# Kernel tuning notes

Measured on AMD Instinct MI355X. Metric: run time of the kernel, lower is better.

## Reference

```python
import jax, jax.numpy as jnp
import numpy as np
import math

D = 512
B, L = 8, 2048
EPS = 1e-5

def setup_inputs() -> dict:
    key = jax.random.key(0)
    ks = jax.random.split(key, 8)
    s = 1.0 / math.sqrt(D)
    x = jax.random.normal(ks[0], (B, L, D), dtype=jnp.float32)
    adj = jax.random.randint(ks[1], (B, L, L), 0, 2, dtype=jnp.int32)
    Wq = jax.random.normal(ks[2], (D, D), dtype=jnp.float32) * s
    Wk = jax.random.normal(ks[3], (D, D), dtype=jnp.float32) * s
    Wv = jax.random.normal(ks[4], (D, D), dtype=jnp.float32) * s
    Wo = jax.random.normal(ks[5], (D, D), dtype=jnp.float32) * s
    bo = jnp.zeros((D,), dtype=jnp.float32)
    gamma = jnp.ones((D,), dtype=jnp.float32)
    beta = jnp.zeros((D,), dtype=jnp.float32)
    return {"x": x, "adj": adj, "Wq": Wq, "Wk": Wk, "Wv": Wv,
            "Wo": Wo, "bo": bo, "gamma": gamma, "beta": beta}

def layer_norm(y, gamma, beta):
    mu = jnp.mean(y, axis=-1, keepdims=True)
    var = jnp.mean(jnp.square(y - mu), axis=-1, keepdims=True)
    return (y - mu) * jax.lax.rsqrt(var + EPS) * gamma + beta

def reference(x, adj, Wq, Wk, Wv, Wo, bo, gamma, beta):
    d_out = Wq.shape[1]
    scale = 1.0 / math.sqrt(d_out)
    Q = x @ Wq                          # [B,L,D]
    K = x @ Wk
    V = x @ Wv
    sc = jnp.einsum('bld,bmd->blm', Q, K) * scale   # [B,L,L]
    mask = adj == 0
    sc = jnp.where(mask, -jnp.inf, sc)
    all_inf = jnp.all(mask, axis=-1, keepdims=True)  # rows with no neighbors
    sc = jnp.where(all_inf, 0.0, sc)                 # -> uniform attention
    w = jax.nn.softmax(sc, axis=-1)                  # dropout off (eval)
    out = jnp.einsum('blm,bmd->bld', w, V)
    y = x + out @ Wo + bo
    return layer_norm(y, gamma, beta)
```

## Files before the change

kernel.cpp:

```cpp
#include <hip/hip_runtime.h>
#include <hip/hip_bf16.h>

typedef short bf16x8 __attribute__((ext_vector_type(8)));
typedef float f32x4  __attribute__((ext_vector_type(4)));
typedef unsigned int u32;

#define LSEQ 2048
#define DDIM 512
#define NBAT 8

__device__ __forceinline__ void gld_lds16(const __hip_bfloat16* g, __hip_bfloat16* l) {
    __builtin_amdgcn_global_load_lds(
        (const __attribute__((address_space(1))) u32*)g,
        (__attribute__((address_space(3))) u32*)l, 16, 0, 0);
}

__global__ void k_cvt_x(const float* __restrict__ x, __hip_bfloat16* __restrict__ xb) {
    size_t i = ((size_t)blockIdx.x * 256 + threadIdx.x) * 4;
    float4 v = *(const float4*)(x + i);
    __hip_bfloat16 h[4] = { __float2bfloat16(v.x), __float2bfloat16(v.y),
                            __float2bfloat16(v.z), __float2bfloat16(v.w) };
    *(short4*)(xb + i) = *(short4*)h;
}

__global__ void k_cvt_w(const float* __restrict__ Wq, const float* __restrict__ Wk,
                        const float* __restrict__ Wv, const float* __restrict__ Wo,
                        __hip_bfloat16* __restrict__ Wtqkv, __hip_bfloat16* __restrict__ Wto) {
    __shared__ float t[32][33];
    int mat = blockIdx.x >> 8;
    int tb  = blockIdx.x & 255;
    int tk  = tb >> 4, tn = tb & 15;
    const float* W = (mat == 0) ? Wq : (mat == 1) ? Wk : (mat == 2) ? Wv : Wo;
    int c  = threadIdx.x & 31;
    int r0 = threadIdx.x >> 5;
#pragma unroll
    for (int i = 0; i < 4; ++i) {
        int r = r0 + i * 8;
        t[r][c] = W[(size_t)(tk * 32 + r) * 512 + tn * 32 + c];
    }
    __syncthreads();
    __hip_bfloat16* dst = (mat < 3) ? (Wtqkv + (size_t)mat * 512 * 512) : Wto;
#pragma unroll
    for (int i = 0; i < 4; ++i) {
        int n = r0 + i * 8;
        dst[(size_t)(tn * 32 + n) * 512 + tk * 32 + c] = __float2bfloat16(t[c][n]);
    }
}

__global__ __launch_bounds__(256, 2)
void k_gemm_qkv(const __hip_bfloat16* __restrict__ A, const __hip_bfloat16* __restrict__ Bt,
                __hip_bfloat16* __restrict__ Q, __hip_bfloat16* __restrict__ Kb,
                __hip_bfloat16* __restrict__ Vt) {
    __shared__ __hip_bfloat16 As[128][32], Bs[128][32];
    const int tid = threadIdx.x, lane = tid & 63, w = tid >> 6;
    const int l15 = lane & 15, l4 = lane >> 4;
    const int mt = blockIdx.x, nt = blockIdx.y;
    const int wr = (w >> 1) * 64, wc = (w & 1) * 64;
    const int sr = lane >> 2, so = (lane & 3) * 8;
    f32x4 acc[4][4] = {};

#pragma unroll 1
    for (int kt = 0; kt < 16; ++kt) {
        __syncthreads();
#pragma unroll
        for (int i = 0; i < 2; ++i) {
            int r0 = w * 32 + i * 16;
            gld_lds16(A  + (size_t)(mt * 128 + r0 + sr) * 512 + kt * 32 + so, &As[r0][0]);
            gld_lds16(Bt + (size_t)(nt * 128 + r0 + sr) * 512 + kt * 32 + so, &Bs[r0][0]);
        }
        __syncthreads();
        bf16x8 af[4], bfr[4];
#pragma unroll
        for (int i = 0; i < 4; ++i)
            af[i] = *(const bf16x8*)(&As[wr + 16 * i + l15][l4 * 8]);
#pragma unroll
        for (int j = 0; j < 4; ++j)
            bfr[j] = *(const bf16x8*)(&Bs[wc + 16 * j + l15][l4 * 8]);
        __builtin_amdgcn_s_setprio(1);
#pragma unroll
        for (int i = 0; i < 4; ++i)
#pragma unroll
            for (int j = 0; j < 4; ++j)
                acc[i][j] = __builtin_amdgcn_mfma_f32_16x16x32_bf16(af[i], bfr[j], acc[i][j], 0, 0, 0);
        __builtin_amdgcn_s_setprio(0);
    }
    const int which = (nt * 128) >> 9;
#pragma unroll
    for (int i = 0; i < 4; ++i) {
#pragma unroll
        for (int r = 0; r < 4; ++r) {
            int grow = mt * 128 + wr + 16 * i + (l4 << 2) + r;
#pragma unroll
            for (int j = 0; j < 4; ++j) {
                int gcol = nt * 128 + wc + 16 * j + l15;
                int cc = gcol & 511;
                __hip_bfloat16 h = __float2bfloat16(acc[i][j][r]);
                if (which == 0)      Q [(size_t)grow * 512 + cc] = h;
                else if (which == 1) Kb[(size_t)grow * 512 + cc] = h;
                else {
                    int b = grow >> 11, m = grow & 2047;
                    Vt[((size_t)b * 512 + cc) * 2048 + m] = h;
                }
            }
        }
    }
}

__global__ __launch_bounds__(512, 2)
void k_attn(const __hip_bfloat16* __restrict__ Q, const __hip_bfloat16* __restrict__ Kg,
            const __hip_bfloat16* __restrict__ Vt, const int* __restrict__ adj,
            __hip_bfloat16* __restrict__ P0, __hip_bfloat16* __restrict__ P1,
            float* __restrict__ mlb) {
    __shared__ __hip_bfloat16 Kl[2][32][520];
    __shared__ __hip_bfloat16 Vl[2][512][32];
    __shared__ __hip_bfloat16 Pl[8][16][40];
    const int tid = threadIdx.x, lane = tid & 63, w = tid >> 6;
    const int l15 = lane & 15, l4 = lane >> 4;
    const int b = blockIdx.x & 7, qt = (blockIdx.x >> 3) & 15, s = blockIdx.x >> 7;
    const float scale = 0.04419417382415922f;
    __hip_bfloat16* __restrict__ Op = s ? P1 : P0;

    const __hip_bfloat16* kbase = Kg + ((size_t)b * LSEQ + s * 1024) * 512;
    const __hip_bfloat16* vbase = Vt + (size_t)b * 512 * 2048 + s * 1024;
    const int* abase = adj + ((size_t)b * LSEQ + qt * 128 + w * 16 + l4 * 4) * LSEQ + s * 1024 + l15;
    const int vsr = lane >> 2, vso = (lane & 3) * 8;

    bf16x8 qf[16];
    {
        const __hip_bfloat16* qp = Q + ((size_t)b * LSEQ + qt * 128 + w * 16 + l15) * 512;
#pragma unroll
        for (int ks = 0; ks < 16; ++ks)
            qf[ks] = *(const bf16x8*)(qp + ks * 32 + l4 * 8);
    }
    f32x4 acc[32];
#pragma unroll
    for (int n = 0; n < 32; ++n) acc[n] = (f32x4){0.f, 0.f, 0.f, 0.f};
    float m_[4] = {-1e30f, -1e30f, -1e30f, -1e30f};
    float l_[4] = {0.f, 0.f, 0.f, 0.f};

    int adjv[8];
    {
#pragma unroll
        for (int i = 0; i < 4; ++i) {
            int r = w + i * 8;
            gld_lds16(kbase + (size_t)r * 512 + lane * 8, &Kl[0][r][0]);
        }
#pragma unroll
        for (int i = 0; i < 4; ++i) {
            int r0 = (w * 4 + i) * 16;
            gld_lds16(vbase + (size_t)(r0 + vsr) * 2048 + vso, &Vl[0][r0][0]);
        }
#pragma unroll
        for (int r = 0; r < 4; ++r)
#pragma unroll
            for (int n = 0; n < 2; ++n)
                adjv[r * 2 + n] = abase[(size_t)r * LSEQ + n * 16];
    }
    __syncthreads();

#pragma unroll 1
    for (int t = 0; t < 32; ++t) {
        const int cur = t & 1, nxt = cur ^ 1;
        unsigned amask = 0;
#pragma unroll
        for (int r = 0; r < 4; ++r)
#pragma unroll
            for (int n = 0; n < 2; ++n)
                amask |= (adjv[r * 2 + n] != 0 ? 1u : 0u) << (n * 4 + r);
        if (t < 31) {
            const __hip_bfloat16* kp = kbase + (size_t)(t + 1) * 32 * 512;
#pragma unroll
            for (int i = 0; i < 4; ++i) {
                int r = w + i * 8;
                gld_lds16(kp + (size_t)r * 512 + lane * 8, &Kl[nxt][r][0]);
            }
            const __hip_bfloat16* vp = vbase + (t + 1) * 32;
#pragma unroll
            for (int i = 0; i < 4; ++i) {
                int r0 = (w * 4 + i) * 16;
                gld_lds16(vp + (size_t)(r0 + vsr) * 2048 + vso, &Vl[nxt][r0][0]);
            }
            const int* ap = abase + (t + 1) * 32;
#pragma unroll
            for (int r = 0; r < 4; ++r)
#pragma unroll
                for (int n = 0; n < 2; ++n)
                    adjv[r * 2 + n] = ap[(size_t)r * LSEQ + n * 16];
        }
        f32x4 sa[2];
#pragma unroll
        for (int n = 0; n < 2; ++n) sa[n] = (f32x4){0.f, 0.f, 0.f, 0.f};
        __builtin_amdgcn_s_setprio(1);
#pragma unroll
        for (int ks = 0; ks < 16; ++ks) {
#pragma unroll
            for (int n = 0; n < 2; ++n) {
                bf16x8 bk = *(const bf16x8*)(&Kl[cur][n * 16 + l15][ks * 32 + l4 * 8]);
                sa[n] = __builtin_amdgcn_mfma_f32_16x16x32_bf16(qf[ks], bk, sa[n], 0, 0, 0);
            }
        }
        __builtin_amdgcn_s_setprio(0);
        float mx[4];
#pragma unroll
        for (int r = 0; r < 4; ++r) {
            float v = -1e30f;
#pragma unroll
            for (int n = 0; n < 2; ++n)
                if ((amask >> (n * 4 + r)) & 1) v = fmaxf(v, sa[n][r] * scale);
            v = fmaxf(v, __shfl_xor(v, 1));
            v = fmaxf(v, __shfl_xor(v, 2));
            v = fmaxf(v, __shfl_xor(v, 4));
            v = fmaxf(v, __shfl_xor(v, 8));
            mx[r] = v;
        }
        float rs[4];
        bool need = false;
#pragma unroll
        for (int r = 0; r < 4; ++r) {
            rs[r] = 1.f;
            if (mx[r] > m_[r] + 8.f) { rs[r] = __expf(m_[r] - mx[r]); m_[r] = mx[r]; }
            l_[r] *= rs[r];
            need |= (rs[r] != 1.f);
        }
        if (need) {
#pragma unroll
            for (int n = 0; n < 32; ++n) {
                acc[n][0] *= rs[0]; acc[n][1] *= rs[1];
                acc[n][2] *= rs[2]; acc[n][3] *= rs[3];
            }
        }
#pragma unroll
        for (int n = 0; n < 2; ++n)
#pragma unroll
            for (int r = 0; r < 4; ++r) {
                float p = ((amask >> (n * 4 + r)) & 1) ? __expf(sa[n][r] * scale - m_[r]) : 0.f;
                sa[n][r] = p;
            }
#pragma unroll
        for (int r = 0; r < 4; ++r) {
            float sm = sa[0][r] + sa[1][r];
            sm += __shfl_xor(sm, 1);
            sm += __shfl_xor(sm, 2);
            sm += __shfl_xor(sm, 4);
            sm += __shfl_xor(sm, 8);
            l_[r] += sm;
        }
#pragma unroll
        for (int n = 0; n < 2; ++n)
#pragma unroll
            for (int r = 0; r < 4; ++r)
                Pl[w][l4 * 4 + r][n * 16 + l15] = __float2bfloat16(sa[n][r]);
        {
            bf16x8 pf = *(const bf16x8*)(&Pl[w][l15][l4 * 8]);
            __builtin_amdgcn_s_setprio(1);
#pragma unroll
            for (int n = 0; n < 32; ++n) {
                bf16x8 bv = *(const bf16x8*)(&Vl[cur][n * 16 + l15][l4 * 8]);
                acc[n] = __builtin_amdgcn_mfma_f32_16x16x32_bf16(pf, bv, acc[n], 0, 0, 0);
            }
            __builtin_amdgcn_s_setprio(0);
        }
        __syncthreads();
    }
#pragma unroll
    for (int r = 0; r < 4; ++r) {
        size_t row = (size_t)b * LSEQ + qt * 128 + w * 16 + l4 * 4 + r;
#pragma unroll
        for (int n = 0; n < 32; ++n)
            Op[row * 512 + n * 16 + l15] = __float2bfloat16(acc[n][r]);
        if (l15 == 0) {
            mlb[((size_t)s * 16384 + row) * 2 + 0] = m_[r];
            mlb[((size_t)s * 16384 + row) * 2 + 1] = l_[r];
        }
    }
}

__global__ void k_combine(const __hip_bfloat16* p0, const __hip_bfloat16* __restrict__ p1,
                          const float* __restrict__ mlb, __hip_bfloat16* outp) {
    size_t idx = (size_t)blockIdx.x * 256 + threadIdx.x;
    size_t row = idx >> 6;
    int    c8  = (int)(idx & 63) * 8;
    float m0 = mlb[row * 2 + 0],             l0 = mlb[row * 2 + 1];
    float m1 = mlb[(16384 + row) * 2 + 0],   l1 = mlb[(16384 + row) * 2 + 1];
    float M  = fmaxf(m0, m1);
    float e0 = __expf(m0 - M), e1 = __expf(m1 - M);
    float den = l0 * e0 + l1 * e1;
    float inv = (den > 0.f) ? 1.f / den : 0.f;
    bf16x8 a = *(const bf16x8*)(p0 + row * 512 + c8);
    bf16x8 c = *(const bf16x8*)(p1 + row * 512 + c8);
    __hip_bfloat16 o[8];
#pragma unroll
    for (int k = 0; k < 8; ++k) {
        float fa = __bfloat162float(*(const __hip_bfloat16*)&((short*)&a)[k]);
        float fc = __bfloat162float(*(const __hip_bfloat16*)&((short*)&c)[k]);
        o[k] = __float2bfloat16((fa * e0 + fc * e1) * inv);
    }
    *(bf16x8*)(outp + row * 512 + c8) = *(bf16x8*)o;
}

__global__ __launch_bounds__(256, 2)
void k_gemm_out(const __hip_bfloat16* __restrict__ A, const __hip_bfloat16* __restrict__ Bt,
                const float* __restrict__ x, const float* __restrict__ bo,
                float* __restrict__ Y) {
    __shared__ __hip_bfloat16 As[128][32], Bs[128][32];
    const int tid = threadIdx.x, lane = tid & 63, w = tid >> 6;
    const int l15 = lane & 15, l4 = lane >> 4;
    const int mt = blockIdx.x, nt = blockIdx.y;
    const int wr = (w >> 1) * 64, wc = (w & 1) * 64;
    const int sr = lane >> 2, so = (lane & 3) * 8;
    f32x4 acc[4][4] = {};

#pragma unroll 1
    for (int kt = 0; kt < 16; ++kt) {
        __syncthreads();
#pragma unroll
        for (int i = 0; i < 2; ++i) {
            int r0 = w * 32 + i * 16;
            gld_lds16(A  + (size_t)(mt * 128 + r0 + sr) * 512 + kt * 32 + so, &As[r0][0]);
            gld_lds16(Bt + (size_t)(nt * 128 + r0 + sr) * 512 + kt * 32 + so, &Bs[r0][0]);
        }
        __syncthreads();
        bf16x8 af[4], bfr[4];
#pragma unroll
        for (int i = 0; i < 4; ++i)
            af[i] = *(const bf16x8*)(&As[wr + 16 * i + l15][l4 * 8]);
#pragma unroll
        for (int j = 0; j < 4; ++j)
            bfr[j] = *(const bf16x8*)(&Bs[wc + 16 * j + l15][l4 * 8]);
        __builtin_amdgcn_s_setprio(1);
#pragma unroll
        for (int i = 0; i < 4; ++i)
#pragma unroll
            for (int j = 0; j < 4; ++j)
                acc[i][j] = __builtin_amdgcn_mfma_f32_16x16x32_bf16(af[i], bfr[j], acc[i][j], 0, 0, 0);
        __builtin_amdgcn_s_setprio(0);
    }
#pragma unroll
    for (int i = 0; i < 4; ++i) {
#pragma unroll
        for (int r = 0; r < 4; ++r) {
            size_t grow = (size_t)mt * 128 + wr + 16 * i + (l4 << 2) + r;
#pragma unroll
            for (int j = 0; j < 4; ++j) {
                int gcol = nt * 128 + wc + 16 * j + l15;
                Y[grow * 512 + gcol] = x[grow * 512 + gcol] + acc[i][j][r] + bo[gcol];
            }
        }
    }
}

__global__ void k_ln(float* __restrict__ Y, const float* __restrict__ gamma,
                     const float* __restrict__ beta, float* __restrict__ out) {
    size_t row = blockIdx.x;
    int lane = threadIdx.x;
    float* y = Y + row * 512;
    float4 v0 = *(const float4*)(y + lane * 8);
    float4 v1 = *(const float4*)(y + lane * 8 + 4);
    float s = v0.x + v0.y + v0.z + v0.w + v1.x + v1.y + v1.z + v1.w;
    float q = v0.x * v0.x + v0.y * v0.y + v0.z * v0.z + v0.w * v0.w +
              v1.x * v1.x + v1.y * v1.y + v1.z * v1.z + v1.w * v1.w;
#pragma unroll
    for (int off = 1; off < 64; off <<= 1) {
        s += __shfl_xor(s, off);
        q += __shfl_xor(q, off);
    }
    float mu = s * (1.f / 512.f);
    float var = q * (1.f / 512.f) - mu * mu;
    float rsd = rsqrtf(var + 1e-5f);
    float o[8] = {v0.x, v0.y, v0.z, v0.w, v1.x, v1.y, v1.z, v1.w};
#pragma unroll
    for (int k = 0; k < 8; ++k) {
        int c = lane * 8 + k;
        o[k] = (o[k] - mu) * rsd * gamma[c] + beta[c];
    }
    *(float4*)(out + row * 512 + lane * 8)     = (float4){o[0], o[1], o[2], o[3]};
    *(float4*)(out + row * 512 + lane * 8 + 4) = (float4){o[4], o[5], o[6], o[7]};
}

extern "C" void kernel_launch(void* const* d_in, const int* in_sizes, int n_in,
                              void* d_out, int out_size, void* d_ws, size_t ws_size,
                              hipStream_t stream) {
    const float* x     = (const float*)d_in[0];
    const int*   adj   = (const int*)d_in[1];
    const float* Wq    = (const float*)d_in[2];
    const float* Wk    = (const float*)d_in[3];
    const float* Wv    = (const float*)d_in[4];
    const float* Wo    = (const float*)d_in[5];
    const float* bo    = (const float*)d_in[6];
    const float* gamma = (const float*)d_in[7];
    const float* beta  = (const float*)d_in[8];
    float* out = (float*)d_out;

    char* ws = (char*)d_ws;
    const size_t SZ_ROWS = (size_t)NBAT * LSEQ;
    __hip_bfloat16* xb    = (__hip_bfloat16*)(ws);
    __hip_bfloat16* Wtqkv = (__hip_bfloat16*)(ws + 16777216);
    __hip_bfloat16* Wto   = (__hip_bfloat16*)(ws + 18350080);
    __hip_bfloat16* Qb    = (__hip_bfloat16*)(ws + 18874368);
    __hip_bfloat16* Kb    = (__hip_bfloat16*)(ws + 35651584);
    __hip_bfloat16* Vtb   = (__hip_bfloat16*)(ws + 52428800);
    __hip_bfloat16* P1    = (__hip_bfloat16*)(ws + 69206016);
    float*          mlb   = (float*)        (ws + 85983232);
    __hip_bfloat16* P0    = xb;
    __hip_bfloat16* Ab    = xb;
    (void)in_sizes; (void)n_in; (void)out_size; (void)ws_size;

    k_cvt_x<<<(SZ_ROWS * DDIM) / (256 * 4), 256, 0, stream>>>(x, xb);
    k_cvt_w<<<1024, 256, 0, stream>>>(Wq, Wk, Wv, Wo, Wtqkv, Wto);
    k_gemm_qkv<<<dim3(128, 12), 256, 0, stream>>>(xb, Wtqkv, Qb, Kb, Vtb);
    k_attn<<<256, 512, 0, stream>>>(Qb, Kb, Vtb, adj, P0, P1, mlb);
    k_combine<<<4096, 256, 0, stream>>>(P0, P1, mlb, Ab);
    k_gemm_out<<<dim3(128, 4), 256, 0, stream>>>(Ab, Wto, x, bo, out);
    k_ln<<<(unsigned)SZ_ROWS, 64, 0, stream>>>(out, gamma, beta, out);
}
```

Before: 249.3 us.

## Switch attention Q/K/V and P to FP8 with swizzled LDS and 64-key tiles

```diff
diff --git a/kernel.cpp b/kernel.cpp
--- a/kernel.cpp
+++ b/kernel.cpp
@@ -4,15 +4,19 @@
 typedef short bf16x8 __attribute__((ext_vector_type(8)));
 typedef float f32x4  __attribute__((ext_vector_type(4)));
 typedef unsigned int u32;
+typedef unsigned char u8;
 
 #define LSEQ 2048
 #define DDIM 512
 #define NBAT 8
 
-__device__ __forceinline__ void gld_lds16(const __hip_bfloat16* g, __hip_bfloat16* l) {
+__device__ __forceinline__ void gld_lds16(const void* g, void* l) {
     __builtin_amdgcn_global_load_lds(
         (const __attribute__((address_space(1))) u32*)g,
         (__attribute__((address_space(3))) u32*)l, 16, 0, 0);
+}
+__device__ __forceinline__ u8 f32_to_fp8(float v) {
+    return (u8)(__builtin_amdgcn_cvt_pk_fp8_f32(v, 0.f, 0, false) & 0xff);
 }
 
 __global__ void k_cvt_x(const float* __restrict__ x, __hip_bfloat16* __restrict__ xb) {
@@ -49,8 +53,7 @@
 
 __global__ __launch_bounds__(256, 2)
 void k_gemm_qkv(const __hip_bfloat16* __restrict__ A, const __hip_bfloat16* __restrict__ Bt,
-                __hip_bfloat16* __restrict__ Q, __hip_bfloat16* __restrict__ Kb,
-                __hip_bfloat16* __restrict__ Vt) {
+                u8* __restrict__ Q, u8* __restrict__ Kb, u8* __restrict__ Vt) {
     __shared__ __hip_bfloat16 As[128][32], Bs[128][32];
     const int tid = threadIdx.x, lane = tid & 63, w = tid >> 6;
     const int l15 = lane & 15, l4 = lane >> 4;
@@ -94,12 +97,12 @@
             for (int j = 0; j < 4; ++j) {
                 int gcol = nt * 128 + wc + 16 * j + l15;
                 int cc = gcol & 511;
-                __hip_bfloat16 h = __float2bfloat16(acc[i][j][r]);
-                if (which == 0)      Q [(size_t)grow * 512 + cc] = h;
-                else if (which == 1) Kb[(size_t)grow * 512 + cc] = h;
+                u8 h8 = f32_to_fp8(acc[i][j][r]);
+                if (which == 0)      Q [(size_t)grow * 512 + cc] = h8;
+                else if (which == 1) Kb[(size_t)grow * 512 + cc] = h8;
                 else {
                     int b = grow >> 11, m = grow & 2047;
-                    Vt[((size_t)b * 512 + cc) * 2048 + m] = h;
+                    Vt[((size_t)b * 512 + cc) * 2048 + m] = h8;
                 }
             }
         }
@@ -107,30 +110,32 @@
 }
 
 __global__ __launch_bounds__(512, 2)
-void k_attn(const __hip_bfloat16* __restrict__ Q, const __hip_bfloat16* __restrict__ Kg,
-            const __hip_bfloat16* __restrict__ Vt, const int* __restrict__ adj,
+void k_attn(const u8* __restrict__ Q, const u8* __restrict__ Kg,
+            const u8* __restrict__ Vt, const int* __restrict__ adj,
             __hip_bfloat16* __restrict__ P0, __hip_bfloat16* __restrict__ P1,
             float* __restrict__ mlb) {
-    __shared__ __hip_bfloat16 Kl[2][32][520];
-    __shared__ __hip_bfloat16 Vl[2][512][32];
-    __shared__ __hip_bfloat16 Pl[8][16][40];
+    __shared__ u8 Kl[2][64 * 512];
+    __shared__ u8 Vl[2][512 * 64];
+    __shared__ u8 Pl[8][16][72];
     const int tid = threadIdx.x, lane = tid & 63, w = tid >> 6;
     const int l15 = lane & 15, l4 = lane >> 4;
     const int b = blockIdx.x & 7, qt = (blockIdx.x >> 3) & 15, s = blockIdx.x >> 7;
     const float scale = 0.04419417382415922f;
     __hip_bfloat16* __restrict__ Op = s ? P1 : P0;
 
-    const __hip_bfloat16* kbase = Kg + ((size_t)b * LSEQ + s * 1024) * 512;
-    const __hip_bfloat16* vbase = Vt + (size_t)b * 512 * 2048 + s * 1024;
+    const u8* kbase = Kg + ((size_t)b * LSEQ + s * 1024) * 512;
+    const u8* vbase = Vt + (size_t)b * 512 * 2048 + s * 1024;
     const int* abase = adj + ((size_t)b * LSEQ + qt * 128 + w * 16 + l4 * 4) * LSEQ + s * 1024 + l15;
-    const int vsr = lane >> 2, vso = (lane & 3) * 8;
-
-    bf16x8 qf[16];
+
+    const int krr = lane >> 5, kcs = lane & 31;
+    const int vdr = lane >> 2, vcs = lane & 3;
+
+    long qf[16];
     {
-        const __hip_bfloat16* qp = Q + ((size_t)b * LSEQ + qt * 128 + w * 16 + l15) * 512;
+        const u8* qp = Q + ((size_t)b * LSEQ + qt * 128 + w * 16 + l15) * 512;
 #pragma unroll
         for (int ks = 0; ks < 16; ++ks)
-            qf[ks] = *(const bf16x8*)(qp + ks * 32 + l4 * 8);
+            qf[ks] = *(const long*)(qp + ks * 32 + l4 * 8);
     }
     f32x4 acc[32];
 #pragma unroll
@@ -138,65 +143,70 @@
     float m_[4] = {-1e30f, -1e30f, -1e30f, -1e30f};
     float l_[4] = {0.f, 0.f, 0.f, 0.f};
 
-    int adjv[8];
+    int adjv[16];
     {
 #pragma unroll
         for (int i = 0; i < 4; ++i) {
-            int r = w + i * 8;
-            gld_lds16(kbase + (size_t)r * 512 + lane * 8, &Kl[0][r][0]);
+            int r0 = w * 8 + i * 2;
+            int r  = r0 + krr;
+            gld_lds16(kbase + (size_t)r * 512 + ((kcs ^ (r & 7)) << 4), &Kl[0][r0 * 512]);
         }
 #pragma unroll
         for (int i = 0; i < 4; ++i) {
-            int r0 = (w * 4 + i) * 16;
-            gld_lds16(vbase + (size_t)(r0 + vsr) * 2048 + vso, &Vl[0][r0][0]);
+            int d0 = (w * 4 + i) * 16;
+            int d  = d0 + vdr;
+            gld_lds16(vbase + (size_t)d * 2048 + ((vcs ^ (d & 3)) << 4), &Vl[0][d0 * 64]);
         }
 #pragma unroll
         for (int r = 0; r < 4; ++r)
 #pragma unroll
-            for (int n = 0; n < 2; ++n)
-                adjv[r * 2 + n] = abase[(size_t)r * LSEQ + n * 16];
+            for (int n = 0; n < 4; ++n)
+                adjv[r * 4 + n] = abase[(size_t)r * LSEQ + n * 16];
     }
     __syncthreads();
 
 #pragma unroll 1
-    for (int t = 0; t < 32; ++t) {
+    for (int t = 0; t < 16; ++t) {
         const int cur = t & 1, nxt = cur ^ 1;
         unsigned amask = 0;
 #pragma unroll
         for (int r = 0; r < 4; ++r)
 #pragma unroll
-            for (int n = 0; n < 2; ++n)
-                amask |= (adjv[r * 2 + n] != 0 ? 1u : 0u) << (n * 4 + r);
-        if (t < 31) {
-            const __hip_bfloat16* kp = kbase + (size_t)(t + 1) * 32 * 512;
+            for (int n = 0; n < 4; ++n)
+                amask |= (adjv[r * 4 + n] != 0 ? 1u : 0u) << (n * 4 + r);
+        if (t < 15) {
+            const u8* kp = kbase + (size_t)(t + 1) * 64 * 512;
 #pragma unroll
             for (int i = 0; i < 4; ++i) {
-                int r = w + i * 8;
-                gld_lds16(kp + (size_t)r * 512 + lane * 8, &Kl[nxt][r][0]);
-            }
-            const __hip_bfloat16* vp = vbase + (t + 1) * 32;
+                int r0 = w * 8 + i * 2;
+                int r  = r0 + krr;
+                gld_lds16(kp + (size_t)r * 512 + ((kcs ^ (r & 7)) << 4), &Kl[nxt][r0 * 512]);
+            }
+            const u8* vp = vbase + (t + 1) * 64;
 #pragma unroll
             for (int i = 0; i < 4; ++i) {
-                int r0 = (w * 4 + i) * 16;
-                gld_lds16(vp + (size_t)(r0 + vsr) * 2048 + vso, &Vl[nxt][r0][0]);
-            }
-            const int* ap = abase + (t + 1) * 32;
+                int d0 = (w * 4 + i) * 16;
+                int d  = d0 + vdr;
+                gld_lds16(vp + (size_t)d * 2048 + ((vcs ^ (d & 3)) << 4), &Vl[nxt][d0 * 64]);
+            }
+            const int* ap = abase + (t + 1) * 64;
 #pragma unroll
             for (int r = 0; r < 4; ++r)
 #pragma unroll
-                for (int n = 0; n < 2; ++n)
-                    adjv[r * 2 + n] = ap[(size_t)r * LSEQ + n * 16];
-        }
-        f32x4 sa[2];
-#pragma unroll
-        for (int n = 0; n < 2; ++n) sa[n] = (f32x4){0.f, 0.f, 0.f, 0.f};
+                for (int n = 0; n < 4; ++n)
+                    adjv[r * 4 + n] = ap[(size_t)r * LSEQ + n * 16];
+        }
+        f32x4 sa[4];
+#pragma unroll
+        for (int n = 0; n < 4; ++n) sa[n] = (f32x4){0.f, 0.f, 0.f, 0.f};
         __builtin_amdgcn_s_setprio(1);
 #pragma unroll
         for (int ks = 0; ks < 16; ++ks) {
 #pragma unroll
-            for (int n = 0; n < 2; ++n) {
-                bf16x8 bk = *(const bf16x8*)(&Kl[cur][n * 16 + l15][ks * 32 + l4 * 8]);
-                sa[n] = __builtin_amdgcn_mfma_f32_16x16x32_bf16(qf[ks], bk, sa[n], 0, 0, 0);
+            for (int n = 0; n < 4; ++n) {
+                int r = n * 16 + l15;
+                long kf = *(const long*)(&Kl[cur][r * 512 + (((2 * ks + (l4 >> 1)) ^ (r & 7)) << 4) + ((l4 & 1) << 3)]);
+                sa[n] = __builtin_amdgcn_mfma_f32_16x16x32_fp8_fp8(qf[ks], kf, sa[n], 0, 0, 0);
             }
         }
         __builtin_amdgcn_s_setprio(0);
@@ -205,7 +215,7 @@
         for (int r = 0; r < 4; ++r) {
             float v = -1e30f;
 #pragma unroll
-            for (int n = 0; n < 2; ++n)
+            for (int n = 0; n < 4; ++n)
                 if ((amask >> (n * 4 + r)) & 1) v = fmaxf(v, sa[n][r] * scale);
             v = fmaxf(v, __shfl_xor(v, 1));
             v = fmaxf(v, __shfl_xor(v, 2));
@@ -218,7 +228,7 @@
 #pragma unroll
         for (int r = 0; r < 4; ++r) {
             rs[r] = 1.f;
-            if (mx[r] > m_[r] + 8.f) { rs[r] = __expf(m_[r] - mx[r]); m_[r] = mx[r]; }
+            if (mx[r] > m_[r] + 5.f) { rs[r] = __expf(m_[r] - mx[r]); m_[r] = mx[r]; }
             l_[r] *= rs[r];
             need |= (rs[r] != 1.f);
         }
@@ -230,36 +240,34 @@
             }
         }
 #pragma unroll
-        for (int n = 0; n < 2; ++n)
+        for (int n = 0; n < 4; ++n)
 #pragma unroll
             for (int r = 0; r < 4; ++r) {
                 float p = ((amask >> (n * 4 + r)) & 1) ? __expf(sa[n][r] * scale - m_[r]) : 0.f;
                 sa[n][r] = p;
+                Pl[w][l4 * 4 + r][n * 16 + l15] = f32_to_fp8(p);
             }
 #pragma unroll
         for (int r = 0; r < 4; ++r) {
-            float sm = sa[0][r] + sa[1][r];
+            float sm = sa[0][r] + sa[1][r] + sa[2][r] + sa[3][r];
             sm += __shfl_xor(sm, 1);
             sm += __shfl_xor(sm, 2);
             sm += __shfl_xor(sm, 4);
             sm += __shfl_xor(sm, 8);
             l_[r] += sm;
         }
-#pragma unroll
-        for (int n = 0; n < 2; ++n)
-#pragma unroll
-            for (int r = 0; r < 4; ++r)
-                Pl[w][l4 * 4 + r][n * 16 + l15] = __float2bfloat16(sa[n][r]);
-        {
-            bf16x8 pf = *(const bf16x8*)(&Pl[w][l15][l4 * 8]);
-            __builtin_amdgcn_s_setprio(1);
+        __builtin_amdgcn_s_setprio(1);
+#pragma unroll
+        for (int ks2 = 0; ks2 < 2; ++ks2) {
+            long pf = *(const long*)(&Pl[w][l15][ks2 * 32 + l4 * 8]);
 #pragma unroll
             for (int n = 0; n < 32; ++n) {
-                bf16x8 bv = *(const bf16x8*)(&Vl[cur][n * 16 + l15][l4 * 8]);
-                acc[n] = __builtin_amdgcn_mfma_f32_16x16x32_bf16(pf, bv, acc[n], 0, 0, 0);
-            }
-            __builtin_amdgcn_s_setprio(0);
-        }
+                int d = n * 16 + l15;
+                long vf = *(const long*)(&Vl[cur][d * 64 + (((2 * ks2 + (l4 >> 1)) ^ (d & 3)) << 4) + ((l4 & 1) << 3)]);
+                acc[n] = __builtin_amdgcn_mfma_f32_16x16x32_fp8_fp8(pf, vf, acc[n], 0, 0, 0);
+            }
+        }
+        __builtin_amdgcn_s_setprio(0);
         __syncthreads();
     }
 #pragma unroll
@@ -396,11 +404,11 @@
     __hip_bfloat16* xb    = (__hip_bfloat16*)(ws);
     __hip_bfloat16* Wtqkv = (__hip_bfloat16*)(ws + 16777216);
     __hip_bfloat16* Wto   = (__hip_bfloat16*)(ws + 18350080);
-    __hip_bfloat16* Qb    = (__hip_bfloat16*)(ws + 18874368);
-    __hip_bfloat16* Kb    = (__hip_bfloat16*)(ws + 35651584);
-    __hip_bfloat16* Vtb   = (__hip_bfloat16*)(ws + 52428800);
-    __hip_bfloat16* P1    = (__hip_bfloat16*)(ws + 69206016);
-    float*          mlb   = (float*)        (ws + 85983232);
+    u8*             Qb    = (u8*)            (ws + 18874368);
+    u8*             Kb    = (u8*)            (ws + 27262976);
+    u8*             Vtb   = (u8*)            (ws + 35651584);
+    __hip_bfloat16* P1    = (__hip_bfloat16*)(ws + 44040192);
+    float*          mlb   = (float*)         (ws + 60817408);
     __hip_bfloat16* P0    = xb;
     __hip_bfloat16* Ab    = xb;
     (void)in_sizes; (void)n_in; (void)out_size; (void)ws_size;
```

Result: slower. 269.4 us (+8.0%).

## Fuse split-attention combine, output projection and LayerNorm; swizzle V tile in LDS

Applied to the files above, without the earlier changes.

```diff
diff --git a/kernel.cpp b/kernel.cpp
--- a/kernel.cpp
+++ b/kernel.cpp
@@ -9,10 +9,18 @@
 #define DDIM 512
 #define NBAT 8
 
-__device__ __forceinline__ void gld_lds16(const __hip_bfloat16* g, __hip_bfloat16* l) {
+__device__ __forceinline__ void gld_lds16(const void* g, void* l) {
     __builtin_amdgcn_global_load_lds(
         (const __attribute__((address_space(1))) u32*)g,
         (__attribute__((address_space(3))) u32*)l, 16, 0, 0);
+}
+__device__ __forceinline__ float bf2f(short s) {
+    u32 u = ((u32)(unsigned short)s) << 16;
+    union { u32 u; float f; } c; c.u = u; return c.f;
+}
+__device__ __forceinline__ short f2bf(float f) {
+    __hip_bfloat16 h = __float2bfloat16(f);
+    return *(short*)&h;
 }
 
 __global__ void k_cvt_x(const float* __restrict__ x, __hip_bfloat16* __restrict__ xb) {
@@ -123,7 +131,8 @@
     const __hip_bfloat16* kbase = Kg + ((size_t)b * LSEQ + s * 1024) * 512;
     const __hip_bfloat16* vbase = Vt + (size_t)b * 512 * 2048 + s * 1024;
     const int* abase = adj + ((size_t)b * LSEQ + qt * 128 + w * 16 + l4 * 4) * LSEQ + s * 1024 + l15;
-    const int vsr = lane >> 2, vso = (lane & 3) * 8;
+    const int vsr = lane >> 2;
+    const int vswz = (l4 ^ ((l15 >> 1) & 3)) * 8;
 
     bf16x8 qf[16];
     {
@@ -148,7 +157,8 @@
 #pragma unroll
         for (int i = 0; i < 4; ++i) {
             int r0 = (w * 4 + i) * 16;
-            gld_lds16(vbase + (size_t)(r0 + vsr) * 2048 + vso, &Vl[0][r0][0]);
+            int d  = r0 + vsr;
+            gld_lds16(vbase + (size_t)d * 2048 + (((lane & 3) ^ ((d >> 1) & 3)) << 3), &Vl[0][r0][0]);
         }
 #pragma unroll
         for (int r = 0; r < 4; ++r)
@@ -178,7 +188,8 @@
 #pragma unroll
             for (int i = 0; i < 4; ++i) {
                 int r0 = (w * 4 + i) * 16;
-                gld_lds16(vp + (size_t)(r0 + vsr) * 2048 + vso, &Vl[nxt][r0][0]);
+                int d  = r0 + vsr;
+                gld_lds16(vp + (size_t)d * 2048 + (((lane & 3) ^ ((d >> 1) & 3)) << 3), &Vl[nxt][r0][0]);
             }
             const int* ap = abase + (t + 1) * 32;
 #pragma unroll
@@ -255,7 +266,7 @@
             __builtin_amdgcn_s_setprio(1);
 #pragma unroll
             for (int n = 0; n < 32; ++n) {
-                bf16x8 bv = *(const bf16x8*)(&Vl[cur][n * 16 + l15][l4 * 8]);
+                bf16x8 bv = *(const bf16x8*)(&Vl[cur][n * 16 + l15][vswz]);
                 acc[n] = __builtin_amdgcn_mfma_f32_16x16x32_bf16(pf, bv, acc[n], 0, 0, 0);
             }
             __builtin_amdgcn_s_setprio(0);
@@ -275,106 +286,121 @@
     }
 }
 
-__global__ void k_combine(const __hip_bfloat16* p0, const __hip_bfloat16* __restrict__ p1,
-                          const float* __restrict__ mlb, __hip_bfloat16* outp) {
-    size_t idx = (size_t)blockIdx.x * 256 + threadIdx.x;
-    size_t row = idx >> 6;
-    int    c8  = (int)(idx & 63) * 8;
-    float m0 = mlb[row * 2 + 0],             l0 = mlb[row * 2 + 1];
-    float m1 = mlb[(16384 + row) * 2 + 0],   l1 = mlb[(16384 + row) * 2 + 1];
-    float M  = fmaxf(m0, m1);
-    float e0 = __expf(m0 - M), e1 = __expf(m1 - M);
-    float den = l0 * e0 + l1 * e1;
-    float inv = (den > 0.f) ? 1.f / den : 0.f;
-    bf16x8 a = *(const bf16x8*)(p0 + row * 512 + c8);
-    bf16x8 c = *(const bf16x8*)(p1 + row * 512 + c8);
-    __hip_bfloat16 o[8];
-#pragma unroll
-    for (int k = 0; k < 8; ++k) {
-        float fa = __bfloat162float(*(const __hip_bfloat16*)&((short*)&a)[k]);
-        float fc = __bfloat162float(*(const __hip_bfloat16*)&((short*)&c)[k]);
-        o[k] = __float2bfloat16((fa * e0 + fc * e1) * inv);
-    }
-    *(bf16x8*)(outp + row * 512 + c8) = *(bf16x8*)o;
-}
-
-__global__ __launch_bounds__(256, 2)
-void k_gemm_out(const __hip_bfloat16* __restrict__ A, const __hip_bfloat16* __restrict__ Bt,
-                const float* __restrict__ x, const float* __restrict__ bo,
-                float* __restrict__ Y) {
-    __shared__ __hip_bfloat16 As[128][32], Bs[128][32];
+__global__ __launch_bounds__(512, 2)
+void k_out_ln(const __hip_bfloat16* __restrict__ p0, const __hip_bfloat16* __restrict__ p1,
+              const float* __restrict__ mlb, const __hip_bfloat16* __restrict__ Bt,
+              const float* __restrict__ x, const float* __restrict__ bo,
+              const float* __restrict__ gamma, const float* __restrict__ beta,
+              float* __restrict__ out) {
+    __shared__ __hip_bfloat16 As[64][32];
+    __shared__ __hip_bfloat16 Bs[512][32];
+    __shared__ float part[64][4][2];
+    __shared__ float lnmv[64][2];
     const int tid = threadIdx.x, lane = tid & 63, w = tid >> 6;
     const int l15 = lane & 15, l4 = lane >> 4;
-    const int mt = blockIdx.x, nt = blockIdx.y;
-    const int wr = (w >> 1) * 64, wc = (w & 1) * 64;
-    const int sr = lane >> 2, so = (lane & 3) * 8;
-    f32x4 acc[4][4] = {};
+    const int mt = blockIdx.x;
+    const int rs = (w >> 2) * 32, cbs = (w & 3) * 128;
+    f32x4 acc[2][8] = {};
+
+    float c0 = 0.f, c1 = 0.f;
+    size_t grow_s = 0;
+    int ko = (tid & 3) * 8;
+    if (tid < 256) {
+        int arow = tid >> 2;
+        grow_s = (size_t)mt * 64 + arow;
+        float m0 = mlb[grow_s * 2], l0 = mlb[grow_s * 2 + 1];
+        float m1 = mlb[(16384 + grow_s) * 2], l1 = mlb[(16384 + grow_s) * 2 + 1];
+        float M  = fmaxf(m0, m1);
+        float e0 = __expf(m0 - M), e1 = __expf(m1 - M);
+        float den = l0 * e0 + l1 * e1;
+        float inv = (den > 0.f) ? 1.f / den : 0.f;
+        c0 = e0 * inv; c1 = e1 * inv;
+    }
 
 #pragma unroll 1
     for (int kt = 0; kt < 16; ++kt) {
         __syncthreads();
 #pragma unroll
-        for (int i = 0; i < 2; ++i) {
-            int r0 = w * 32 + i * 16;
-            gld_lds16(A  + (size_t)(mt * 128 + r0 + sr) * 512 + kt * 32 + so, &As[r0][0]);
-            gld_lds16(Bt + (size_t)(nt * 128 + r0 + sr) * 512 + kt * 32 + so, &Bs[r0][0]);
+        for (int i = 0; i < 4; ++i) {
+            int br = w * 64 + i * 16;
+            gld_lds16(Bt + (size_t)(br + (lane >> 2)) * 512 + kt * 32 + (lane & 3) * 8, &Bs[br][0]);
+        }
+        if (tid < 256) {
+            bf16x8 a0 = *(const bf16x8*)(p0 + grow_s * 512 + kt * 32 + ko);
+            bf16x8 a1 = *(const bf16x8*)(p1 + grow_s * 512 + kt * 32 + ko);
+            short h[8];
+#pragma unroll
+            for (int k = 0; k < 8; ++k)
+                h[k] = f2bf(c0 * bf2f(a0[k]) + c1 * bf2f(a1[k]));
+            *(bf16x8*)(&As[tid >> 2][ko]) = *(bf16x8*)h;
         }
         __syncthreads();
-        bf16x8 af[4], bfr[4];
-#pragma unroll
-        for (int i = 0; i < 4; ++i)
-            af[i] = *(const bf16x8*)(&As[wr + 16 * i + l15][l4 * 8]);
-#pragma unroll
-        for (int j = 0; j < 4; ++j)
-            bfr[j] = *(const bf16x8*)(&Bs[wc + 16 * j + l15][l4 * 8]);
+        bf16x8 af[2], bfr[8];
+#pragma unroll
+        for (int i = 0; i < 2; ++i)
+            af[i] = *(const bf16x8*)(&As[rs + 16 * i + l15][l4 * 8]);
+#pragma unroll
+        for (int j = 0; j < 8; ++j)
+            bfr[j] = *(const bf16x8*)(&Bs[cbs + 16 * j + l15][l4 * 8]);
         __builtin_amdgcn_s_setprio(1);
 #pragma unroll
-        for (int i = 0; i < 4; ++i)
-#pragma unroll
-            for (int j = 0; j < 4; ++j)
+        for (int i = 0; i < 2; ++i)
+#pragma unroll
+            for (int j = 0; j < 8; ++j)
                 acc[i][j] = __builtin_amdgcn_mfma_f32_16x16x32_bf16(af[i], bfr[j], acc[i][j], 0, 0, 0);
         __builtin_amdgcn_s_setprio(0);
     }
 #pragma unroll
-    for (int i = 0; i < 4; ++i) {
-#pragma unroll
-        for (int r = 0; r < 4; ++r) {
-            size_t grow = (size_t)mt * 128 + wr + 16 * i + (l4 << 2) + r;
-#pragma unroll
-            for (int j = 0; j < 4; ++j) {
-                int gcol = nt * 128 + wc + 16 * j + l15;
-                Y[grow * 512 + gcol] = x[grow * 512 + gcol] + acc[i][j][r] + bo[gcol];
-            }
-        }
-    }
-}
-
-__global__ void k_ln(float* __restrict__ Y, const float* __restrict__ gamma,
-                     const float* __restrict__ beta, float* __restrict__ out) {
-    size_t row = blockIdx.x;
-    int lane = threadIdx.x;
-    float* y = Y + row * 512;
-    float4 v0 = *(const float4*)(y + lane * 8);
-    float4 v1 = *(const float4*)(y + lane * 8 + 4);
-    float s = v0.x + v0.y + v0.z + v0.w + v1.x + v1.y + v1.z + v1.w;
-    float q = v0.x * v0.x + v0.y * v0.y + v0.z * v0.z + v0.w * v0.w +
-              v1.x * v1.x + v1.y * v1.y + v1.z * v1.z + v1.w * v1.w;
-#pragma unroll
-    for (int off = 1; off < 64; off <<= 1) {
-        s += __shfl_xor(s, off);
-        q += __shfl_xor(q, off);
-    }
-    float mu = s * (1.f / 512.f);
-    float var = q * (1.f / 512.f) - mu * mu;
-    float rsd = rsqrtf(var + 1e-5f);
-    float o[8] = {v0.x, v0.y, v0.z, v0.w, v1.x, v1.y, v1.z, v1.w};
-#pragma unroll
-    for (int k = 0; k < 8; ++k) {
-        int c = lane * 8 + k;
-        o[k] = (o[k] - mu) * rsd * gamma[c] + beta[c];
-    }
-    *(float4*)(out + row * 512 + lane * 8)     = (float4){o[0], o[1], o[2], o[3]};
-    *(float4*)(out + row * 512 + lane * 8 + 4) = (float4){o[4], o[5], o[6], o[7]};
+    for (int i = 0; i < 2; ++i) {
+#pragma unroll
+        for (int r = 0; r < 4; ++r) {
+            int rl = rs + 16 * i + 4 * l4 + r;
+            size_t grow = (size_t)mt * 64 + rl;
+            float s = 0.f, q = 0.f;
+#pragma unroll
+            for (int j = 0; j < 8; ++j) {
+                int col = cbs + 16 * j + l15;
+                float y = x[grow * 512 + col] + acc[i][j][r] + bo[col];
+                acc[i][j][r] = y;
+                s += y; q += y * y;
+            }
+            s += __shfl_xor(s, 1); q += __shfl_xor(q, 1);
+            s += __shfl_xor(s, 2); q += __shfl_xor(q, 2);
+            s += __shfl_xor(s, 4); q += __shfl_xor(q, 4);
+            s += __shfl_xor(s, 8); q += __shfl_xor(q, 8);
+            if (l15 == 0) { part[rl][w & 3][0] = s; part[rl][w & 3][1] = q; }
+        }
+    }
+    __syncthreads();
+    if (tid < 64) {
+        float S  = part[tid][0][0] + part[tid][1][0] + part[tid][2][0] + part[tid][3][0];
+        float Q2 = part[tid][0][1] + part[tid][1][1] + part[tid][2][1] + part[tid][3][1];
+        float mu = S * (1.f / 512.f);
+        float var = Q2 * (1.f / 512.f) - mu * mu;
+        lnmv[tid][0] = mu;
+        lnmv[tid][1] = rsqrtf(var + 1e-5f);
+    }
+    __syncthreads();
+    float gm[8], bt2[8];
+#pragma unroll
+    for (int j = 0; j < 8; ++j) {
+        int col = cbs + 16 * j + l15;
+        gm[j] = gamma[col]; bt2[j] = beta[col];
+    }
+#pragma unroll
+    for (int i = 0; i < 2; ++i) {
+#pragma unroll
+        for (int r = 0; r < 4; ++r) {
+            int rl = rs + 16 * i + 4 * l4 + r;
+            size_t grow = (size_t)mt * 64 + rl;
+            float mu = lnmv[rl][0], rsd = lnmv[rl][1];
+#pragma unroll
+            for (int j = 0; j < 8; ++j) {
+                int col = cbs + 16 * j + l15;
+                out[grow * 512 + col] = (acc[i][j][r] - mu) * rsd * gm[j] + bt2[j];
+            }
+        }
+    }
 }
 
 extern "C" void kernel_launch(void* const* d_in, const int* in_sizes, int n_in,
@@ -400,16 +426,13 @@
     __hip_bfloat16* Kb    = (__hip_bfloat16*)(ws + 35651584);
     __hip_bfloat16* Vtb   = (__hip_bfloat16*)(ws + 52428800);
     __hip_bfloat16* P1    = (__hip_bfloat16*)(ws + 69206016);
-    float*          mlb   = (float*)        (ws + 85983232);
+    float*          mlb   = (float*)         (ws + 85983232);
     __hip_bfloat16* P0    = xb;
-    __hip_bfloat16* Ab    = xb;
     (void)in_sizes; (void)n_in; (void)out_size; (void)ws_size;
 
     k_cvt_x<<<(SZ_ROWS * DDIM) / (256 * 4), 256, 0, stream>>>(x, xb);
     k_cvt_w<<<1024, 256, 0, stream>>>(Wq, Wk, Wv, Wo, Wtqkv, Wto);
     k_gemm_qkv<<<dim3(128, 12), 256, 0, stream>>>(xb, Wtqkv, Qb, Kb, Vtb);
     k_attn<<<256, 512, 0, stream>>>(Qb, Kb, Vtb, adj, P0, P1, mlb);
-    k_combine<<<4096, 256, 0, stream>>>(P0, P1, mlb, Ab);
-    k_gemm_out<<<dim3(128, 4), 256, 0, stream>>>(Ab, Wto, x, bo, out);
-    k_ln<<<(unsigned)SZ_ROWS, 64, 0, stream>>>(out, gamma, beta, out);
-}
+    k_out_ln<<<256, 512, 0, stream>>>(P0, P1, mlb, Wto, x, bo, gamma, beta, out);
+}
```

New measurement: 237.9 us. -4.6%, faster.
